# Kernel optimization log

Hardware: AMD Instinct MI355X
Metric: run time of the kernel (lower is better)

## Reference

```python
import jax, jax.numpy as jnp
import numpy as np

D = 128  # feature = hidden = output dim (residuals force equality)


def setup_inputs() -> dict:
    key = jax.random.key(0)
    kx, k1, k2, kr = jax.random.split(key, 4)
    B, N = 8, 2048
    x = jax.random.normal(kx, (B, N, D), dtype=jnp.float32)
    w1 = jax.random.normal(k1, (D, D), dtype=jnp.float32)
    w2 = jax.random.normal(k2, (D, D), dtype=jnp.float32)
    wr = jax.random.normal(kr, (D, D), dtype=jnp.float32)
    return {"x": x, "w1": w1, "w2": w2, "wr": wr}


def reference(x, w1, w2, wr):
    # bilinear scores: [B, N, N]
    R = jnp.einsum('bnf,fg,bmg->bnm', x, wr, x)
    R = jax.nn.softmax(R, axis=2)
    # layer 1: relu(R @ x @ w1 + x)
    x = jax.nn.relu(jnp.einsum('bnm,bmf->bnf', R, x) @ w1 + x)
    # layer 2: relu(R @ x @ w2 + x)
    x = jax.nn.relu(jnp.einsum('bnm,bmf->bnf', R, x) @ w2 + x)
    return x[:, 0, :]
```

## Files before the change

### kernel.cpp

```cpp
#include <hip/hip_runtime.h>
#include <stdint.h>

typedef float  f32x4 __attribute__((ext_vector_type(4)));
typedef short  s16x8 __attribute__((ext_vector_type(8)));
typedef unsigned int u32;
typedef u32    u32x2 __attribute__((ext_vector_type(2)));
typedef u32    u32x4 __attribute__((ext_vector_type(4)));
typedef unsigned short u16;

#define MFMA16(a,b,c) __builtin_amdgcn_mfma_f32_16x16x32_bf16((a),(b),(c),0,0,0)

__device__ __forceinline__ u16 f2bf(float f){
  u32 u = __float_as_uint(f);
  return (u16)((u + 0x7fffu + ((u >> 16) & 1u)) >> 16);
}
__device__ __forceinline__ float bf2f(u16 h){ return __uint_as_float(((u32)h) << 16); }
__device__ __forceinline__ u32 pack2bf(float a, float b){ return (u32)f2bf(a) | ((u32)f2bf(b) << 16); }
__device__ __forceinline__ u32 packtrunc(float a, float b){
  return (__float_as_uint(a) >> 16) | (__float_as_uint(b) & 0xffff0000u);
}
__device__ __forceinline__ f32x4 f4zero(){ f32x4 z; z[0]=0.f; z[1]=0.f; z[2]=0.f; z[3]=0.f; return z; }
__device__ __forceinline__ s16x8 mk8(u32 a, u32 b, u32 c, u32 d){
  u32x4 w; w[0]=a; w[1]=b; w[2]=c; w[3]=d;
  return __builtin_bit_cast(s16x8, w);
}

__device__ __forceinline__ void async16(const void* g, void* l){
  __builtin_amdgcn_global_load_lds(
      (const __attribute__((address_space(1))) unsigned int*)g,
      (__attribute__((address_space(3))) unsigned int*)l, 16, 0, 0);
}

__global__ __launch_bounds__(256) void k_prep(
    const float* __restrict__ x, const float* __restrict__ wr, const float* __restrict__ w1,
    u16* __restrict__ xh, u16* __restrict__ xl, u16* __restrict__ Xt,
    u16* __restrict__ w1t, float* __restrict__ S0, float* __restrict__ maxpart,
    u16* __restrict__ yh, u16* __restrict__ yl)
{
  __shared__ __align__(16) char smem[65536];
  const int tid = threadIdx.x, bid = blockIdx.x;

  if (bid < 1024){
    float (*xs)[132] = (float(*)[132])smem;
    const long base = (long)bid * 2048;
#pragma unroll
    for (int k = 0; k < 8; k++){
      int idx = tid + k*256;
      float v = x[base + idx];
      xs[idx>>7][idx&127] = v;
      u16 h = f2bf(v);
      xh[base+idx] = h;
      xl[base+idx] = f2bf(v - bf2f(h));
    }
    __syncthreads();
    const int b  = bid >> 7;
    const int n0 = (bid & 127) * 16;
    const int nn = tid & 15, d0 = tid >> 4;
#pragma unroll
    for (int d = 0; d < 8; d++){
      int dd = d0 + d*16;
      Xt[(long)b*262144 + (long)dd*2048 + n0 + nn] = f2bf(xs[nn][dd]);
    }
  } else if (bid < 1032){
    const int base = (bid - 1024) * 2048;
#pragma unroll
    for (int k = 0; k < 8; k++){
      int idx = base + k*256 + tid;
      int c = idx >> 7, f = idx & 127;
      w1t[idx] = f2bf(w1[f*128 + c]);
    }
  } else if (bid < 1096){
    float* x0s = (float*)smem;
    float* ys  = x0s + 128;
    float* red = ys + 128;
    const int jj = bid - 1032;
    const int b = jj >> 3, j = jj & 7;
    if (tid < 128) x0s[tid] = x[(long)b*262144 + tid];
    __syncthreads();
    if (tid < 128){
      float a = 0.f;
      for (int f = 0; f < 128; f++) a += x0s[f] * wr[f*128 + tid];
      ys[tid] = a;
    }
    __syncthreads();
    const int m = j*256 + tid;
    const float4* xr = (const float4*)(x + ((long)b*2048 + m)*128);
    const float4* yv = (const float4*)ys;
    float acc = 0.f;
#pragma unroll
    for (int f = 0; f < 32; f++){
      float4 a = xr[f], c = yv[f];
      acc += a.x*c.x + a.y*c.y + a.z*c.z + a.w*c.w;
    }
    S0[b*2048 + m] = acc;
    red[tid] = acc;
    __syncthreads();
    for (int sft = 128; sft > 0; sft >>= 1){
      if (tid < sft) red[tid] = fmaxf(red[tid], red[tid + sft]);
      __syncthreads();
    }
    if (tid == 0) maxpart[jj] = red[0];
  } else {
    u16* sbh = (u16*)smem;
    u16* sbl = sbh + 16384;
    {
      const int c = tid & 127, f0 = (tid >> 7) * 64;
      const int key = (c & 7) << 4;
#pragma unroll
      for (int fi = 0; fi < 64; fi += 2){
        int f = f0 + fi;
        float v0 = wr[f*128 + c], v1 = wr[(f+1)*128 + c];
        u16 h0 = f2bf(v0), h1 = f2bf(v1);
        u32 hw = (u32)h0 | ((u32)h1 << 16);
        u32 lw = (u32)f2bf(v0 - bf2f(h0)) | ((u32)f2bf(v1 - bf2f(h1)) << 16);
        int byte = c*256 + ((((2*f) & ~15) ^ key) + ((2*f) & 15));
        *(u32*)((char*)sbh + byte) = hw;
        *(u32*)((char*)sbl + byte) = lw;
      }
    }
    __syncthreads();
    const int w = tid >> 6, lane = tid & 63, lr = lane & 15, g = lane >> 4;
    const long rowbase = (long)(bid - 1096)*128 + w*32;
    s16x8 ah[2][4], al[2][4];
#pragma unroll
    for (int rh = 0; rh < 2; rh++)
#pragma unroll
      for (int kc = 0; kc < 4; kc++){
        long r = rowbase + rh*16 + lr;
        const float4* px = (const float4*)(x + r*128 + kc*32 + g*8);
        float4 a = px[0], bV = px[1];
        u32 hh0, hh1, hh2, hh3, ll0, ll1, ll2, ll3;
        { u16 p=f2bf(a.x), q=f2bf(a.y); hh0=(u32)p|((u32)q<<16);
          ll0=(u32)f2bf(a.x-bf2f(p))|((u32)f2bf(a.y-bf2f(q))<<16); }
        { u16 p=f2bf(a.z), q=f2bf(a.w); hh1=(u32)p|((u32)q<<16);
          ll1=(u32)f2bf(a.z-bf2f(p))|((u32)f2bf(a.w-bf2f(q))<<16); }
        { u16 p=f2bf(bV.x), q=f2bf(bV.y); hh2=(u32)p|((u32)q<<16);
          ll2=(u32)f2bf(bV.x-bf2f(p))|((u32)f2bf(bV.y-bf2f(q))<<16); }
        { u16 p=f2bf(bV.z), q=f2bf(bV.w); hh3=(u32)p|((u32)q<<16);
          ll3=(u32)f2bf(bV.z-bf2f(p))|((u32)f2bf(bV.w-bf2f(q))<<16); }
        ah[rh][kc] = mk8(hh0,hh1,hh2,hh3);
        al[rh][kc] = mk8(ll0,ll1,ll2,ll3);
      }
    f32x4 acc[2][8];
#pragma unroll
    for (int rh = 0; rh < 2; rh++)
#pragma unroll
      for (int cg = 0; cg < 8; cg++) acc[rh][cg] = f4zero();
    const int swz = (lr & 7) << 4;
#pragma unroll
    for (int cg = 0; cg < 8; cg++){
      const int rowt = (cg*16 + lr) * 256;
#pragma unroll
      for (int kc = 0; kc < 4; kc++){
        int boff = rowt + ((kc*64 + g*16) ^ swz);
        s16x8 bh = *(const s16x8*)((const char*)sbh + boff);
        s16x8 bl = *(const s16x8*)((const char*)sbl + boff);
#pragma unroll
        for (int rh = 0; rh < 2; rh++){
          acc[rh][cg] = MFMA16(ah[rh][kc], bh, acc[rh][cg]);
          acc[rh][cg] = MFMA16(al[rh][kc], bh, acc[rh][cg]);
          acc[rh][cg] = MFMA16(ah[rh][kc], bl, acc[rh][cg]);
        }
      }
    }
#pragma unroll
    for (int rh = 0; rh < 2; rh++)
#pragma unroll
      for (int cg = 0; cg < 8; cg++)
#pragma unroll
        for (int r = 0; r < 4; r++){
          long q = rowbase + rh*16 + 4*g + r;
          int  c = cg*16 + lr;
          float v = acc[rh][cg][r] * 1.4426950408889634f;
          u16 h = f2bf(v);
          yh[q*128 + c] = h;
          yl[q*128 + c] = f2bf(v - bf2f(h));
        }
  }
}

__global__ __launch_bounds__(512) void k_flash(
    const u16* __restrict__ xh, const u16* __restrict__ xl, const u16* __restrict__ Xt,
    const u16* __restrict__ yh, const u16* __restrict__ yl,
    u16* __restrict__ Opart, float* __restrict__ mpart, float* __restrict__ lpart,
    int KS, int kslog)
{
  __shared__ __align__(16) char lds[49152];
  const int tid = threadIdx.x, bid = blockIdx.x;
  const int b     = bid & 7;
  const int inner = bid >> 3;
  const int s     = inner & (KS - 1);
  const int qbl   = inner >> kslog;
  const int qb    = b*16 + qbl;
  const int nspan = 2048 >> kslog;
  const int kv0   = s * nspan;
  const int ntiles = nspan >> 5;
  const int w = tid >> 6, lane = tid & 63, lr = lane & 15, g = lane >> 4;
  const long qrow = (long)qb*128 + w*16;

  const int soff = w*1024 + lane*16;
  const int sswo = soff ^ (((soff >> 8) & 7) << 4);
  const int trow = soff >> 6;
  const int tsrc = trow*4096 + ((soff & 63) ^ ((trow & 3) << 4));
  const int bS0 = lr*256 + (( 0 + g*16) ^ ((lr & 7) << 4));
  const int bS1 = lr*256 + (( 64 + g*16) ^ ((lr & 7) << 4));
  const int bS2 = lr*256 + ((128 + g*16) ^ ((lr & 7) << 4));
  const int bS3 = lr*256 + ((192 + g*16) ^ ((lr & 7) << 4));
  const int bPV = lr*64 + ((g*16) ^ ((lr & 3) << 4));

  s16x8 byh[4], byl[4];
#pragma unroll
  for (int kc = 0; kc < 4; kc++){
    long r = qrow + lr;
    byh[kc] = *(const s16x8*)(yh + r*128 + kc*32 + g*8);
    byl[kc] = *(const s16x8*)(yl + r*128 + kc*32 + g*8);
  }

  f32x4 o[8];
#pragma unroll
  for (int dg = 0; dg < 8; dg++) o[dg] = f4zero();
  float mrun = -1e30f, lrun = 0.f;

  const char* gxh  = (const char*)xh + ((long)b*2048 + kv0)*256;
  const char* gxl  = (const char*)xl + ((long)b*2048 + kv0)*256;
  const char* gxtb = (const char*)(Xt + (long)b*262144 + kv0);

  auto stage = [&](int bufi, int t){
    char* dst = lds + bufi*8192 + w*1024;
    async16(gxh  + (long)t*8192 + sswo, dst);
    async16(gxl  + (long)t*8192 + sswo, dst + 16384);
    async16(gxtb + (long)t*64   + tsrc, dst + 32768);
  };

  stage(0, 0);
  __syncthreads();

  for (int t = 0; t < ntiles; t++){
    const int cur = t & 1;
    if (t + 1 < ntiles) stage(cur ^ 1, t + 1);
    const char* pb = lds + cur*8192;
    const char* a0 = pb + bS0;
    const char* a1 = pb + bS1;
    const char* a2 = pb + bS2;
    const char* a3 = pb + bS3;

    f32x4 sacc[2];
    sacc[0] = f4zero(); sacc[1] = f4zero();
    __builtin_amdgcn_s_setprio(1);
#pragma unroll
    for (int ch = 0; ch < 2; ch++){
      const int co = ch*4096;
      s16x8 fh, fl;
      fh = *(const s16x8*)(a0 + co); fl = *(const s16x8*)(a0 + 16384 + co);
      sacc[ch] = MFMA16(fh, byh[0], sacc[ch]);
      sacc[ch] = MFMA16(fl, byh[0], sacc[ch]);
      sacc[ch] = MFMA16(fh, byl[0], sacc[ch]);
      fh = *(const s16x8*)(a1 + co); fl = *(const s16x8*)(a1 + 16384 + co);
      sacc[ch] = MFMA16(fh, byh[1], sacc[ch]);
      sacc[ch] = MFMA16(fl, byh[1], sacc[ch]);
      sacc[ch] = MFMA16(fh, byl[1], sacc[ch]);
      fh = *(const s16x8*)(a2 + co); fl = *(const s16x8*)(a2 + 16384 + co);
      sacc[ch] = MFMA16(fh, byh[2], sacc[ch]);
      sacc[ch] = MFMA16(fl, byh[2], sacc[ch]);
      sacc[ch] = MFMA16(fh, byl[2], sacc[ch]);
      fh = *(const s16x8*)(a3 + co); fl = *(const s16x8*)(a3 + 16384 + co);
      sacc[ch] = MFMA16(fh, byh[3], sacc[ch]);
      sacc[ch] = MFMA16(fl, byh[3], sacc[ch]);
      sacc[ch] = MFMA16(fh, byl[3], sacc[ch]);
    }
    __builtin_amdgcn_s_setprio(0);

    float cm = fmaxf(fmaxf(fmaxf(sacc[0][0], sacc[0][1]),
                           fmaxf(sacc[0][2], sacc[0][3])),
                     fmaxf(fmaxf(sacc[1][0], sacc[1][1]),
                           fmaxf(sacc[1][2], sacc[1][3])));
    cm = fmaxf(cm, __shfl_xor(cm, 16, 64));
    cm = fmaxf(cm, __shfl_xor(cm, 32, 64));
    if (__any(cm > mrun + 8.f)){
      float mn = fmaxf(mrun, cm);
      float sc = exp2f(mrun - mn);
#pragma unroll
      for (int dg = 0; dg < 8; dg++)
#pragma unroll
        for (int r = 0; r < 4; r++) o[dg][r] *= sc;
      lrun *= sc;
      mrun = mn;
    }
    float p[2][4];
#pragma unroll
    for (int ch = 0; ch < 2; ch++)
#pragma unroll
      for (int r = 0; r < 4; r++) p[ch][r] = exp2f(sacc[ch][r] - mrun);
    float ls = ((p[0][0] + p[0][1]) + (p[0][2] + p[0][3]))
             + ((p[1][0] + p[1][1]) + (p[1][2] + p[1][3]));
    ls += __shfl_xor(ls, 16, 64);
    ls += __shfl_xor(ls, 32, 64);
    lrun += ls;
    s16x8 bpq;
    {
      u32 pw00 = packtrunc(p[0][0], p[0][1]);
      u32 pw01 = packtrunc(p[0][2], p[0][3]);
      u32 pw10 = packtrunc(p[1][0], p[1][1]);
      u32 pw11 = packtrunc(p[1][2], p[1][3]);
      int sA = ((g & 1) << 5) + lr;
      int sB = sA + 16;
      u32 a0s = (u32)__shfl((int)pw00, sA, 64);
      u32 a1s = (u32)__shfl((int)pw01, sA, 64);
      u32 a2s = (u32)__shfl((int)pw10, sA, 64);
      u32 a3s = (u32)__shfl((int)pw11, sA, 64);
      u32 b0s = (u32)__shfl((int)pw00, sB, 64);
      u32 b1s = (u32)__shfl((int)pw01, sB, 64);
      u32 b2s = (u32)__shfl((int)pw10, sB, 64);
      u32 b3s = (u32)__shfl((int)pw11, sB, 64);
      bool hi = (g >= 2);
      bpq = mk8(hi ? a2s : a0s, hi ? a3s : a1s, hi ? b2s : b0s, hi ? b3s : b1s);
    }

    const char* ap = pb + 32768 + bPV;
    __builtin_amdgcn_s_setprio(1);
#pragma unroll
    for (int half = 0; half < 2; half++){
      s16x8 ax[4];
#pragma unroll
      for (int i = 0; i < 4; i++)
        ax[i] = *(const s16x8*)(ap + (half*4 + i)*1024);
#pragma unroll
      for (int i = 0; i < 4; i++)
        o[half*4 + i] = MFMA16(ax[i], bpq, o[half*4 + i]);
    }
    __builtin_amdgcn_s_setprio(0);
    __syncthreads();
  }

  const long pid = bid;
  {
    int lq = w*16 + lr;
#pragma unroll
    for (int dg = 0; dg < 8; dg++){
      u32x2 pw;
      pw[0] = pack2bf(o[dg][0], o[dg][1]);
      pw[1] = pack2bf(o[dg][2], o[dg][3]);
      *(u32x2*)(Opart + pid*16384 + (long)lq*128 + dg*16 + 4*g) = pw;
    }
    if (g == 0){
      mpart[pid*128 + lq] = mrun;
      lpart[pid*128 + lq] = lrun;
    }
  }
}

__global__ __launch_bounds__(256) void k_mergeL1(
    const u16* __restrict__ Opart, const float* __restrict__ mpart, const float* __restrict__ lpart,
    const u16* __restrict__ w1t, const float* __restrict__ x,
    const float* __restrict__ S0, const float* __restrict__ maxpart,
    float* __restrict__ A2p, float* __restrict__ Lj, float* __restrict__ x1r0,
    int KS)
{
  __shared__ u16 sb[16384];
  __shared__ u16 sa[8192];
  __shared__ float eS[64];
  __shared__ float redw[4][128];
  const int tid = threadIdx.x, bid = blockIdx.x;
  const int bb = bid >> 5;
#pragma unroll
  for (int k = 0; k < 8; k++){
    int off = (tid + k*256)*16;
    int row = off >> 8;
    *(s16x8*)((char*)sb + (off ^ ((row & 7) << 4))) = *(const s16x8*)((const char*)w1t + off);
  }
  if (tid < 64){
    float M = -1e30f;
#pragma unroll
    for (int jj = 0; jj < 8; jj++) M = fmaxf(M, maxpart[bb*8 + jj]);
    eS[tid] = __expf(S0[bb*2048 + (bid & 31)*64 + tid] - M);
  }
  const long R0 = (long)bid*64;
#pragma unroll
  for (int k = 0; k < 4; k++){
    int gidx = tid + k*256;
    int lrow = gidx >> 4, gcol = gidx & 15;
    long R = R0 + lrow;
    int qb = (int)(R >> 7), r = (int)(R & 127);
    int pbase = qb >> 4, qblk = qb & 15;
    float m = -1e30f;
    for (int s = 0; s < KS; s++){
      long pid = (long)((qblk*KS + s)*8 + pbase);
      m = fmaxf(m, mpart[pid*128 + r]);
    }
    float ls = 0.f;
    float a0=0.f,a1=0.f,a2=0.f,a3=0.f,a4=0.f,a5=0.f,a6=0.f,a7=0.f;
    for (int s = 0; s < KS; s++){
      long pid = (long)((qblk*KS + s)*8 + pbase);
      float wgt = exp2f(mpart[pid*128 + r] - m);
      ls += lpart[pid*128 + r] * wgt;
      u32x4 v = *(const u32x4*)(Opart + pid*16384 + (long)r*128 + gcol*8);
      a0 += bf2f((u16)(v[0] & 0xffff)) * wgt;  a1 += bf2f((u16)(v[0] >> 16)) * wgt;
      a2 += bf2f((u16)(v[1] & 0xffff)) * wgt;  a3 += bf2f((u16)(v[1] >> 16)) * wgt;
      a4 += bf2f((u16)(v[2] & 0xffff)) * wgt;  a5 += bf2f((u16)(v[2] >> 16)) * wgt;
      a6 += bf2f((u16)(v[3] & 0xffff)) * wgt;  a7 += bf2f((u16)(v[3] >> 16)) * wgt;
    }
    float inv = 1.f / ls;
    u32x4 pw;
    pw[0] = pack2bf(a0*inv, a1*inv); pw[1] = pack2bf(a2*inv, a3*inv);
    pw[2] = pack2bf(a4*inv, a5*inv); pw[3] = pack2bf(a6*inv, a7*inv);
    int off = lrow*256 + gcol*16;
    *(u32x4*)((char*)sa + (off ^ ((lrow & 7) << 4))) = pw;
  }
  __syncthreads();
  const int w = tid >> 6, lane = tid & 63, lr = lane & 15, g = lane >> 4;
  const long rowbase = R0 + w*16;
  s16x8 aa[4];
#pragma unroll
  for (int kc = 0; kc < 4; kc++){
    int lrow = w*16 + lr;
    aa[kc] = *(const s16x8*)((const char*)sa +
               (lrow*256 + ((kc*64 + g*16) ^ ((lrow & 7) << 4))));
  }
  f32x4 acc[8];
#pragma unroll
  for (int cg = 0; cg < 8; cg++) acc[cg] = f4zero();
  const int swz = (lr & 7) << 4;
#pragma unroll
  for (int cg = 0; cg < 8; cg++){
    const int rowt = (cg*16 + lr)*256;
#pragma unroll
    for (int kc = 0; kc < 4; kc++){
      s16x8 bV = *(const s16x8*)((const char*)sb + rowt + ((kc*64 + g*16) ^ swz));
      acc[cg] = MFMA16(aa[kc], bV, acc[cg]);
    }
  }
  const float e0 = eS[w*16 + 4*g + 0];
  const float e1 = eS[w*16 + 4*g + 1];
  const float e2 = eS[w*16 + 4*g + 2];
  const float e3 = eS[w*16 + 4*g + 3];
  float sA2[8];
#pragma unroll
  for (int cg = 0; cg < 8; cg++){
    int c = cg*16 + lr;
    f32x4 vv;
#pragma unroll
    for (int r = 0; r < 4; r++){
      long q = rowbase + 4*g + r;
      vv[r] = fmaxf(acc[cg][r] + x[q*128 + c], 0.f);
    }
    if (((bid & 31) == 0) && w == 0 && g == 0)
      x1r0[bb*128 + c] = vv[0];
    sA2[cg] = e0*vv[0] + e1*vv[1] + e2*vv[2] + e3*vv[3];
  }
#pragma unroll
  for (int cg = 0; cg < 8; cg++){
    sA2[cg] += __shfl_xor(sA2[cg], 16, 64);
    sA2[cg] += __shfl_xor(sA2[cg], 32, 64);
  }
  if (g == 0){
#pragma unroll
    for (int cg = 0; cg < 8; cg++) redw[w][cg*16 + lr] = sA2[cg];
  }
  __syncthreads();
  if (tid < 128)
    A2p[(long)bid*128 + tid] = redw[0][tid] + redw[1][tid] + redw[2][tid] + redw[3][tid];
  if ((tid >> 6) == 2){
    float v = eS[tid & 63];
    v += __shfl_xor(v, 1, 64);  v += __shfl_xor(v, 2, 64);
    v += __shfl_xor(v, 4, 64);  v += __shfl_xor(v, 8, 64);
    v += __shfl_xor(v, 16, 64); v += __shfl_xor(v, 32, 64);
    if ((tid & 63) == 0) Lj[bid] = v;
  }
}

__global__ __launch_bounds__(256) void k_out(
    const float* __restrict__ A2p, const float* __restrict__ Lj,
    const float* __restrict__ w2, const float* __restrict__ x1r0,
    float* __restrict__ out)
{
  __shared__ float a2s[2][128];
  const int tid = threadIdx.x, bid = blockIdx.x;
  const int b0 = bid*2;
  {
    int which = tid >> 7, f = tid & 127;
    int bb = b0 + which;
    float s = 0.f, L = 0.f;
#pragma unroll
    for (int jj = 0; jj < 32; jj++){
      s += A2p[(long)(bb*32 + jj)*128 + f];
      L += Lj[bb*32 + jj];
    }
    a2s[which][f] = s / L;
  }
  __syncthreads();
  const int which = tid >> 7, d = tid & 127;
  const int b = b0 + which;
  float acc = x1r0[b*128 + d];
  for (int f = 0; f < 128; f++)
    acc += a2s[which][f] * w2[f*128 + d];
  out[b*128 + d] = fmaxf(acc, 0.f);
}

extern "C" void kernel_launch(void* const* d_in, const int* in_sizes, int n_in,
                              void* d_out, int out_size, void* d_ws, size_t ws_size,
                              hipStream_t stream)
{
  const float* x  = (const float*)d_in[0];
  const float* w1 = (const float*)d_in[1];
  const float* w2 = (const float*)d_in[2];
  const float* wr = (const float*)d_in[3];
  float* out = (float*)d_out;
  char* ws = (char*)d_ws;

  u16*   xh      = (u16*)  (ws + 0);
  u16*   xl      = (u16*)  (ws + 4194304);
  u16*   Xt      = (u16*)  (ws + 8388608);
  u16*   yh      = (u16*)  (ws + 12582912);
  u16*   yl      = (u16*)  (ws + 16777216);
  u16*   w1t     = (u16*)  (ws + 20971520);
  float* S0      = (float*)(ws + 21004288);
  float* maxpart = (float*)(ws + 21069824);
  float* Lj      = (float*)(ws + 21070848);
  float* A2p     = (float*)(ws + 21071872);
  float* x1r0    = (float*)(ws + 21202944);
  const size_t tail = 21207040;

  int KS = 4, kslog = 2;
  while (KS > 1 && tail + (size_t)KS*4325376ull > ws_size){ KS >>= 1; kslog--; }
  float* mpart = (float*)(ws + tail);
  float* lpart = (float*)(ws + tail + (size_t)KS*65536);
  u16*   Opart = (u16*)  (ws + tail + (size_t)KS*131072);

  k_prep   <<<1224, 256, 0, stream>>>(x, wr, w1, xh, xl, Xt, w1t, S0, maxpart, yh, yl);
  k_flash  <<<128*KS, 512, 0, stream>>>(xh, xl, Xt, yh, yl, Opart, mpart, lpart, KS, kslog);
  k_mergeL1<<<256, 256, 0, stream>>>(Opart, mpart, lpart, w1t, x, S0, maxpart, A2p, Lj, x1r0, KS);
  k_out    <<<4, 256, 0, stream>>>(A2p, Lj, w2, x1r0, out);
}
```

Measured before the change: 88.67 us.

## Interleave split-K partials per row, double merge grid, delay prefetch

Flash-kernel partial outputs and m/l statistics are now stored so that the KS splits for a given query row sit next to each other, which makes the merge kernel's reads contiguous. The merge kernel now handles 32 rows per block with a 2x2 wave split over rows and columns, and its grid grows from 256 to 512 blocks to fill more CUs. The A2p/Lj buffers and the reduction in k_out are resized to match. In the flash loop, the async prefetch of the next tile is moved to after the score MFMAs, which may reduce contention but shortens the window for overlapping the load.

```diff
diff --git a/kernel.cpp b/kernel.cpp
--- a/kernel.cpp
+++ b/kernel.cpp
@@ -237,7 +237,6 @@
 
   for (int t = 0; t < ntiles; t++){
     const int cur = t & 1;
-    if (t + 1 < ntiles) stage(cur ^ 1, t + 1);
     const char* pb = lds + cur*8192;
     const char* a0 = pb + bS0;
     const char* a1 = pb + bS1;
@@ -269,6 +268,8 @@
       sacc[ch] = MFMA16(fh, byl[3], sacc[ch]);
     }
     __builtin_amdgcn_s_setprio(0);
+
+    if (t + 1 < ntiles) stage(cur ^ 1, t + 1);
 
     float cm = fmaxf(fmaxf(fmaxf(sacc[0][0], sacc[0][1]),
                            fmaxf(sacc[0][2], sacc[0][3])),
@@ -332,19 +333,20 @@
     __syncthreads();
   }
 
-  const long pid = bid;
   {
     int lq = w*16 + lr;
+    long bi = (long)(qbl*8 + b)*128 + lq;
+    u16* op = Opart + bi*(long)(128 << kslog) + s*128;
 #pragma unroll
     for (int dg = 0; dg < 8; dg++){
       u32x2 pw;
       pw[0] = pack2bf(o[dg][0], o[dg][1]);
       pw[1] = pack2bf(o[dg][2], o[dg][3]);
-      *(u32x2*)(Opart + pid*16384 + (long)lq*128 + dg*16 + 4*g) = pw;
+      *(u32x2*)(op + dg*16 + 4*g) = pw;
     }
     if (g == 0){
-      mpart[pid*128 + lq] = mrun;
-      lpart[pid*128 + lq] = lrun;
+      mpart[bi*KS + s] = mrun;
+      lpart[bi*KS + s] = lrun;
     }
   }
 }
@@ -357,43 +359,42 @@
     int KS)
 {
   __shared__ u16 sb[16384];
-  __shared__ u16 sa[8192];
-  __shared__ float eS[64];
-  __shared__ float redw[4][128];
+  __shared__ u16 sa[4096];
+  __shared__ float eS[32];
+  __shared__ float redw[4][64];
   const int tid = threadIdx.x, bid = blockIdx.x;
-  const int bb = bid >> 5;
+  const int bb   = bid >> 6;
+  const int qbl  = (bid >> 2) & 15;
+  const int rb   = (bid & 3) * 32;
+  const long R0  = (long)bid*32;
 #pragma unroll
   for (int k = 0; k < 8; k++){
     int off = (tid + k*256)*16;
     int row = off >> 8;
     *(s16x8*)((char*)sb + (off ^ ((row & 7) << 4))) = *(const s16x8*)((const char*)w1t + off);
   }
-  if (tid < 64){
+  if (tid < 32){
     float M = -1e30f;
 #pragma unroll
     for (int jj = 0; jj < 8; jj++) M = fmaxf(M, maxpart[bb*8 + jj]);
-    eS[tid] = __expf(S0[bb*2048 + (bid & 31)*64 + tid] - M);
-  }
-  const long R0 = (long)bid*64;
-#pragma unroll
-  for (int k = 0; k < 4; k++){
+    eS[tid] = __expf(S0[bb*2048 + (bid & 63)*32 + tid] - M);
+  }
+#pragma unroll
+  for (int k = 0; k < 2; k++){
     int gidx = tid + k*256;
     int lrow = gidx >> 4, gcol = gidx & 15;
-    long R = R0 + lrow;
-    int qb = (int)(R >> 7), r = (int)(R & 127);
-    int pbase = qb >> 4, qblk = qb & 15;
+    long bi = (long)(qbl*8 + bb)*128 + rb + lrow;
+    const float* mp = mpart + bi*KS;
+    const float* lp = lpart + bi*KS;
     float m = -1e30f;
-    for (int s = 0; s < KS; s++){
-      long pid = (long)((qblk*KS + s)*8 + pbase);
-      m = fmaxf(m, mpart[pid*128 + r]);
-    }
+    for (int s = 0; s < KS; s++) m = fmaxf(m, mp[s]);
     float ls = 0.f;
     float a0=0.f,a1=0.f,a2=0.f,a3=0.f,a4=0.f,a5=0.f,a6=0.f,a7=0.f;
+    const u16* ob = Opart + bi*(long)(KS*128) + gcol*8;
     for (int s = 0; s < KS; s++){
-      long pid = (long)((qblk*KS + s)*8 + pbase);
-      float wgt = exp2f(mpart[pid*128 + r] - m);
-      ls += lpart[pid*128 + r] * wgt;
-      u32x4 v = *(const u32x4*)(Opart + pid*16384 + (long)r*128 + gcol*8);
+      float wgt = exp2f(mp[s] - m);
+      ls += lp[s] * wgt;
+      u32x4 v = *(const u32x4*)(ob + s*128);
       a0 += bf2f((u16)(v[0] & 0xffff)) * wgt;  a1 += bf2f((u16)(v[0] >> 16)) * wgt;
       a2 += bf2f((u16)(v[1] & 0xffff)) * wgt;  a3 += bf2f((u16)(v[1] >> 16)) * wgt;
       a4 += bf2f((u16)(v[2] & 0xffff)) * wgt;  a5 += bf2f((u16)(v[2] >> 16)) * wgt;
@@ -408,63 +409,66 @@
   }
   __syncthreads();
   const int w = tid >> 6, lane = tid & 63, lr = lane & 15, g = lane >> 4;
-  const long rowbase = R0 + w*16;
+  const int rowhalf = w & 1, colhalf = w >> 1;
   s16x8 aa[4];
 #pragma unroll
   for (int kc = 0; kc < 4; kc++){
-    int lrow = w*16 + lr;
+    int lrow = rowhalf*16 + lr;
     aa[kc] = *(const s16x8*)((const char*)sa +
                (lrow*256 + ((kc*64 + g*16) ^ ((lrow & 7) << 4))));
   }
-  f32x4 acc[8];
-#pragma unroll
-  for (int cg = 0; cg < 8; cg++) acc[cg] = f4zero();
+  f32x4 acc[4];
+#pragma unroll
+  for (int cg = 0; cg < 4; cg++) acc[cg] = f4zero();
   const int swz = (lr & 7) << 4;
 #pragma unroll
-  for (int cg = 0; cg < 8; cg++){
-    const int rowt = (cg*16 + lr)*256;
+  for (int cg = 0; cg < 4; cg++){
+    const int c = colhalf*64 + cg*16 + lr;
+    const int rowt = c*256;
 #pragma unroll
     for (int kc = 0; kc < 4; kc++){
       s16x8 bV = *(const s16x8*)((const char*)sb + rowt + ((kc*64 + g*16) ^ swz));
       acc[cg] = MFMA16(aa[kc], bV, acc[cg]);
     }
   }
-  const float e0 = eS[w*16 + 4*g + 0];
-  const float e1 = eS[w*16 + 4*g + 1];
-  const float e2 = eS[w*16 + 4*g + 2];
-  const float e3 = eS[w*16 + 4*g + 3];
-  float sA2[8];
-#pragma unroll
-  for (int cg = 0; cg < 8; cg++){
-    int c = cg*16 + lr;
+  const float e0 = eS[rowhalf*16 + 4*g + 0];
+  const float e1 = eS[rowhalf*16 + 4*g + 1];
+  const float e2 = eS[rowhalf*16 + 4*g + 2];
+  const float e3 = eS[rowhalf*16 + 4*g + 3];
+  float sA2[4];
+#pragma unroll
+  for (int cg = 0; cg < 4; cg++){
+    int c = colhalf*64 + cg*16 + lr;
     f32x4 vv;
 #pragma unroll
     for (int r = 0; r < 4; r++){
-      long q = rowbase + 4*g + r;
+      long q = R0 + rowhalf*16 + 4*g + r;
       vv[r] = fmaxf(acc[cg][r] + x[q*128 + c], 0.f);
     }
-    if (((bid & 31) == 0) && w == 0 && g == 0)
+    if (((bid & 63) == 0) && rowhalf == 0 && g == 0)
       x1r0[bb*128 + c] = vv[0];
     sA2[cg] = e0*vv[0] + e1*vv[1] + e2*vv[2] + e3*vv[3];
   }
 #pragma unroll
-  for (int cg = 0; cg < 8; cg++){
+  for (int cg = 0; cg < 4; cg++){
     sA2[cg] += __shfl_xor(sA2[cg], 16, 64);
     sA2[cg] += __shfl_xor(sA2[cg], 32, 64);
   }
   if (g == 0){
 #pragma unroll
-    for (int cg = 0; cg < 8; cg++) redw[w][cg*16 + lr] = sA2[cg];
+    for (int cg = 0; cg < 4; cg++) redw[w][cg*16 + lr] = sA2[cg];
   }
   __syncthreads();
-  if (tid < 128)
-    A2p[(long)bid*128 + tid] = redw[0][tid] + redw[1][tid] + redw[2][tid] + redw[3][tid];
-  if ((tid >> 6) == 2){
-    float v = eS[tid & 63];
+  if (tid < 128){
+    int cl = tid & 63, pair = (tid >> 6) * 2;
+    A2p[(long)bid*128 + tid] = redw[pair][cl] + redw[pair + 1][cl];
+  }
+  if (w == 2){
+    float v = (lane < 32) ? eS[lane] : 0.f;
     v += __shfl_xor(v, 1, 64);  v += __shfl_xor(v, 2, 64);
     v += __shfl_xor(v, 4, 64);  v += __shfl_xor(v, 8, 64);
     v += __shfl_xor(v, 16, 64); v += __shfl_xor(v, 32, 64);
-    if ((tid & 63) == 0) Lj[bid] = v;
+    if (lane == 0) Lj[bid] = v;
   }
 }
 
@@ -481,9 +485,9 @@
     int bb = b0 + which;
     float s = 0.f, L = 0.f;
 #pragma unroll
-    for (int jj = 0; jj < 32; jj++){
-      s += A2p[(long)(bb*32 + jj)*128 + f];
-      L += Lj[bb*32 + jj];
+    for (int jj = 0; jj < 64; jj++){
+      s += A2p[(long)(bb*64 + jj)*128 + f];
+      L += Lj[bb*64 + jj];
     }
     a2s[which][f] = s / L;
   }
@@ -516,9 +520,9 @@
   float* S0      = (float*)(ws + 21004288);
   float* maxpart = (float*)(ws + 21069824);
   float* Lj      = (float*)(ws + 21070848);
-  float* A2p     = (float*)(ws + 21071872);
-  float* x1r0    = (float*)(ws + 21202944);
-  const size_t tail = 21207040;
+  float* A2p     = (float*)(ws + 21072896);
+  float* x1r0    = (float*)(ws + 21335040);
+  const size_t tail = 21339136;
 
   int KS = 4, kslog = 2;
   while (KS > 1 && tail + (size_t)KS*4325376ull > ws_size){ KS >>= 1; kslog--; }
@@ -528,6 +532,6 @@
 
   k_prep   <<<1224, 256, 0, stream>>>(x, wr, w1, xh, xl, Xt, w1t, S0, maxpart, yh, yl);
   k_flash  <<<128*KS, 512, 0, stream>>>(xh, xl, Xt, yh, yl, Opart, mpart, lpart, KS, kslog);
-  k_mergeL1<<<256, 256, 0, stream>>>(Opart, mpart, lpart, w1t, x, S0, maxpart, A2p, Lj, x1r0, KS);
+  k_mergeL1<<<512, 256, 0, stream>>>(Opart, mpart, lpart, w1t, x, S0, maxpart, A2p, Lj, x1r0, KS);
   k_out    <<<4, 256, 0, stream>>>(A2p, Lj, w2, x1r0, out);
 }
```

Result: faster. 82.88 us (-6.5%).
